# Kernel optimization log

Measured on AMD Instinct MI355X. Metric: run time of the kernel, lower is better.

## Reference

```python
import jax, jax.numpy as jnp
import numpy as np

E, T, H, I = 32, 512, 2048, 768


def setup_inputs() -> dict:
    key = jax.random.key(0)
    k1, k2, k3, k4 = jax.random.split(key, 4)
    scale = 1.0 / np.sqrt(H)
    return {
        "routed_input": jax.random.normal(k1, (E, T, H), dtype=jnp.float32),
        "gate_proj": jax.random.normal(k2, (E, I, H), dtype=jnp.float32) * scale,
        "up_proj": jax.random.normal(k3, (E, I, H), dtype=jnp.float32) * scale,
        "down_proj": jax.random.normal(k4, (E, H, I), dtype=jnp.float32) * scale,
    }


def reference(routed_input, gate_proj, up_proj, down_proj):
    # routed_input: [E, T, H]; per-expert SwiGLU MLP, concat over experts.
    gate = jnp.einsum("eth,eih->eti", routed_input, gate_proj)
    up = jnp.einsum("eth,eih->eti", routed_input, up_proj)
    hidden = jax.nn.silu(gate) * up  # [E, T, I]
    out = jnp.einsum("eti,ehi->eth", hidden, down_proj)  # [E, T, H]
    return out.reshape(E * T, H)
```

## Files before the change

### kernel.cpp

```cpp
#include <hip/hip_runtime.h>


#define NE 32
#define NT 512
#define NH 2048
#define NI 768

typedef short        short8  __attribute__((ext_vector_type(8)));
typedef float        floatx4 __attribute__((ext_vector_type(4)));
typedef unsigned int uintx2  __attribute__((ext_vector_type(2)));

__device__ __forceinline__ unsigned int cvt_pk_bf16(float lo, float hi) {
    unsigned int r;
    asm("v_cvt_pk_bf16_f32 %0, %1, %2" : "=v"(r) : "v"(lo), "v"(hi));
    return r;
}

__device__ __forceinline__ uintx2 pack4(floatx4 v) {
    uintx2 r;
    r[0] = cvt_pk_bf16(v[0], v[1]);
    r[1] = cvt_pk_bf16(v[2], v[3]);
    return r;
}

__device__ __forceinline__ ushort f2bf(float f) {
    union { float f; unsigned int u; } v; v.f = f;
    unsigned int r = v.u + 0x7fffu + ((v.u >> 16) & 1u);
    return (ushort)(r >> 16);
}

__global__ __launch_bounds__(256) void moe_gateup(
    const float* __restrict__ rin, const float* __restrict__ gate,
    const float* __restrict__ up, ushort* __restrict__ hidden)
{
    __shared__ ushort As[128][40];
    __shared__ ushort Bgs[128][40];
    __shared__ ushort Bus[128][40];

    const int bid = blockIdx.x;
    const int wg  = (bid & 7) * (768 / 8) + (bid >> 3);
    const int e   = wg / 24;
    const int rem = wg % 24;
    const int ti  = rem % 6;
    const int tm  = rem / 6;

    const int tid  = threadIdx.x;
    const int lane = tid & 63;
    const int wave = tid >> 6;
    const int wr = wave >> 1, wc = wave & 1;

    const float* Ab = rin  + (size_t)e * NT * NH + (size_t)(tm * 128) * NH;
    const float* Gb = gate + (size_t)e * NI * NH + (size_t)(ti * 128) * NH;
    const float* Ub = up   + (size_t)e * NI * NH + (size_t)(ti * 128) * NH;

    const int srow = tid >> 3;
    const int scol = (tid & 7) * 4;

    floatx4 accg[4][4], accu[4][4];
    #pragma unroll
    for (int m = 0; m < 4; ++m)
        #pragma unroll
        for (int n = 0; n < 4; ++n) {
            accg[m][n] = (floatx4)0.f;
            accu[m][n] = (floatx4)0.f;
        }

    const int frow = lane & 15;
    const int kofs = (lane >> 4) * 8;
    const int KT = NH / 32;

    floatx4 pa[4], pg[4], pu[4];
    #pragma unroll
    for (int r = 0; r < 4; ++r) {
        const size_t off = (size_t)(srow + r * 32) * NH + scol;
        pa[r] = *(const floatx4*)(Ab + off);
        pg[r] = *(const floatx4*)(Gb + off);
        pu[r] = *(const floatx4*)(Ub + off);
    }

    for (int kt = 0; kt < KT; ++kt) {
        __builtin_amdgcn_s_barrier();
        #pragma unroll
        for (int r = 0; r < 4; ++r) {
            const int row = srow + r * 32;
            *(uintx2*)&As [row][scol] = pack4(pa[r]);
            *(uintx2*)&Bgs[row][scol] = pack4(pg[r]);
            *(uintx2*)&Bus[row][scol] = pack4(pu[r]);
        }
        if (kt + 1 < KT) {
            const int k0 = (kt + 1) * 32 + scol;
            #pragma unroll
            for (int r = 0; r < 4; ++r) {
                const size_t off = (size_t)(srow + r * 32) * NH + k0;
                pa[r] = *(const floatx4*)(Ab + off);
                pg[r] = *(const floatx4*)(Gb + off);
                pu[r] = *(const floatx4*)(Ub + off);
            }
        }
        asm volatile("s_waitcnt lgkmcnt(0)" ::: "memory");
        __builtin_amdgcn_s_barrier();

        short8 af[4], gf[4], uf[4];
        #pragma unroll
        for (int m = 0; m < 4; ++m)
            af[m] = *(const short8*)&As[wr * 64 + m * 16 + frow][kofs];
        #pragma unroll
        for (int n = 0; n < 4; ++n) {
            gf[n] = *(const short8*)&Bgs[wc * 64 + n * 16 + frow][kofs];
            uf[n] = *(const short8*)&Bus[wc * 64 + n * 16 + frow][kofs];
        }
        #pragma unroll
        for (int m = 0; m < 4; ++m)
            #pragma unroll
            for (int n = 0; n < 4; ++n) {
                accg[m][n] = __builtin_amdgcn_mfma_f32_16x16x32_bf16(
                    af[m], gf[n], accg[m][n], 0, 0, 0);
                accu[m][n] = __builtin_amdgcn_mfma_f32_16x16x32_bf16(
                    af[m], uf[n], accu[m][n], 0, 0, 0);
            }
    }

    const int ccol  = lane & 15;
    const int crow0 = (lane >> 4) * 4;
    const size_t hbase = ((size_t)e * NT + (size_t)tm * 128) * NI + ti * 128;
    #pragma unroll
    for (int m = 0; m < 4; ++m)
        #pragma unroll
        for (int n = 0; n < 4; ++n)
            #pragma unroll
            for (int j = 0; j < 4; ++j) {
                const float g = accg[m][n][j];
                const float u = accu[m][n][j];
                const float h = (g / (1.f + __expf(-g))) * u;
                const int row = wr * 64 + m * 16 + crow0 + j;
                const int col = wc * 64 + n * 16 + ccol;
                hidden[hbase + (size_t)row * NI + col] = f2bf(h);
            }
}

__global__ __launch_bounds__(256) void moe_down(
    const ushort* __restrict__ hidden, const float* __restrict__ down,
    float* __restrict__ out)
{
    __shared__ ushort As[128][40];
    __shared__ ushort Bs[128][40];

    const int bid = blockIdx.x;
    const int wg  = (bid & 7) * (2048 / 8) + (bid >> 3);
    const int e   = wg >> 6;
    const int rem = wg & 63;
    const int tn  = rem & 15;
    const int tm  = rem >> 4;

    const int tid  = threadIdx.x;
    const int lane = tid & 63;
    const int wave = tid >> 6;
    const int wr = wave >> 1, wc = wave & 1;

    const ushort* Ab = hidden + ((size_t)e * NT + (size_t)tm * 128) * NI;
    const float*  Bb = down + (size_t)e * NH * NI + (size_t)(tn * 128) * NI;

    const int a_row = tid >> 2;
    const int a_col = (tid & 3) * 8;
    const int srow = tid >> 3;
    const int scol = (tid & 7) * 4;

    floatx4 acc[4][4];
    #pragma unroll
    for (int m = 0; m < 4; ++m)
        #pragma unroll
        for (int n = 0; n < 4; ++n) acc[m][n] = (floatx4)0.f;

    const int frow = lane & 15;
    const int kofs = (lane >> 4) * 8;
    const int KT = NI / 32;

    short8 pha0, pha1;
    floatx4 pb[4];
    pha0 = *(const short8*)(Ab + (size_t)a_row * NI + a_col);
    pha1 = *(const short8*)(Ab + (size_t)(a_row + 64) * NI + a_col);
    #pragma unroll
    for (int r = 0; r < 4; ++r)
        pb[r] = *(const floatx4*)(Bb + (size_t)(srow + r * 32) * NI + scol);

    for (int kt = 0; kt < KT; ++kt) {
        __builtin_amdgcn_s_barrier();
        *(short8*)&As[a_row][a_col]      = pha0;
        *(short8*)&As[a_row + 64][a_col] = pha1;
        #pragma unroll
        for (int r = 0; r < 4; ++r)
            *(uintx2*)&Bs[srow + r * 32][scol] = pack4(pb[r]);
        if (kt + 1 < KT) {
            const int k0 = (kt + 1) * 32;
            pha0 = *(const short8*)(Ab + (size_t)a_row * NI + k0 + a_col);
            pha1 = *(const short8*)(Ab + (size_t)(a_row + 64) * NI + k0 + a_col);
            #pragma unroll
            for (int r = 0; r < 4; ++r)
                pb[r] = *(const floatx4*)(Bb + (size_t)(srow + r * 32) * NI + k0 + scol);
        }
        asm volatile("s_waitcnt lgkmcnt(0)" ::: "memory");
        __builtin_amdgcn_s_barrier();

        short8 af[4], bf[4];
        #pragma unroll
        for (int m = 0; m < 4; ++m)
            af[m] = *(const short8*)&As[wr * 64 + m * 16 + frow][kofs];
        #pragma unroll
        for (int n = 0; n < 4; ++n)
            bf[n] = *(const short8*)&Bs[wc * 64 + n * 16 + frow][kofs];
        #pragma unroll
        for (int m = 0; m < 4; ++m)
            #pragma unroll
            for (int n = 0; n < 4; ++n)
                acc[m][n] = __builtin_amdgcn_mfma_f32_16x16x32_bf16(
                    af[m], bf[n], acc[m][n], 0, 0, 0);
    }

    const int ccol  = lane & 15;
    const int crow0 = (lane >> 4) * 4;
    float* Ob = out + ((size_t)e * NT + (size_t)tm * 128) * NH + tn * 128;
    #pragma unroll
    for (int m = 0; m < 4; ++m)
        #pragma unroll
        for (int n = 0; n < 4; ++n)
            #pragma unroll
            for (int j = 0; j < 4; ++j) {
                const int row = wr * 64 + m * 16 + crow0 + j;
                const int col = wc * 64 + n * 16 + ccol;
                Ob[(size_t)row * NH + col] = acc[m][n][j];
            }
}

extern "C" void kernel_launch(void* const* d_in, const int* in_sizes, int n_in,
                              void* d_out, int out_size, void* d_ws, size_t ws_size,
                              hipStream_t stream) {
    const float* rin  = (const float*)d_in[0];
    const float* gate = (const float*)d_in[1];
    const float* up   = (const float*)d_in[2];
    const float* down = (const float*)d_in[3];
    float* out = (float*)d_out;
    ushort* hidden = (ushort*)d_ws;

    dim3 blk(256);
    moe_gateup<<<dim3(768), blk, 0, stream>>>(rin, gate, up, hidden);
    moe_down<<<dim3(2048), blk, 0, stream>>>(hidden, down, out);
}
```

Baseline: 402.6 us.

## Load fp32 tiles directly into LDS via global_load_lds with XOR swizzle

Both GEMM kernels now use global_load_lds to copy fp32 (and bf16 hidden) tiles straight from global memory into LDS, with an XOR column swizzle to avoid bank conflicts. The bf16 conversion moves from the staging store to the fragment read. This removes the register staging and the separate LDS write. The register-level prefetch of the next tile is gone, so each iteration now waits on vmcnt(0) with no overlap of loads and MFMA within a block, and the larger fp32 LDS tiles may cut occupancy. Launch bounds also request 2 blocks per SIMD to recover latency hiding.

```diff
diff --git a/kernel.cpp b/kernel.cpp
--- a/kernel.cpp
+++ b/kernel.cpp
@@ -8,7 +8,12 @@
 
 typedef short        short8  __attribute__((ext_vector_type(8)));
 typedef float        floatx4 __attribute__((ext_vector_type(4)));
-typedef unsigned int uintx2  __attribute__((ext_vector_type(2)));
+typedef __attribute__((address_space(1))) const unsigned int g_u32;
+typedef __attribute__((address_space(3))) unsigned int l_u32;
+
+__device__ __forceinline__ void gl_lds16(const void* g, void* l) {
+    __builtin_amdgcn_global_load_lds((g_u32*)g, (l_u32*)l, 16, 0, 0);
+}
 
 __device__ __forceinline__ unsigned int cvt_pk_bf16(float lo, float hi) {
     unsigned int r;
@@ -16,11 +21,13 @@
     return r;
 }
 
-__device__ __forceinline__ uintx2 pack4(floatx4 v) {
-    uintx2 r;
-    r[0] = cvt_pk_bf16(v[0], v[1]);
-    r[1] = cvt_pk_bf16(v[2], v[3]);
-    return r;
+__device__ __forceinline__ short8 frag8(floatx4 x0, floatx4 x1) {
+    union { unsigned int u[4]; short8 s; } t;
+    t.u[0] = cvt_pk_bf16(x0[0], x0[1]);
+    t.u[1] = cvt_pk_bf16(x0[2], x0[3]);
+    t.u[2] = cvt_pk_bf16(x1[0], x1[1]);
+    t.u[3] = cvt_pk_bf16(x1[2], x1[3]);
+    return t.s;
 }
 
 __device__ __forceinline__ ushort f2bf(float f) {
@@ -29,13 +36,13 @@
     return (ushort)(r >> 16);
 }
 
-__global__ __launch_bounds__(256) void moe_gateup(
+__global__ __launch_bounds__(256, 2) void moe_gateup(
     const float* __restrict__ rin, const float* __restrict__ gate,
     const float* __restrict__ up, ushort* __restrict__ hidden)
 {
-    __shared__ ushort As[128][40];
-    __shared__ ushort Bgs[128][40];
-    __shared__ ushort Bus[128][40];
+    __shared__ float As[128][32];
+    __shared__ float Gs[128][32];
+    __shared__ float Us[128][32];
 
     const int bid = blockIdx.x;
     const int wg  = (bid & 7) * (768 / 8) + (bid >> 3);
@@ -53,8 +60,8 @@
     const float* Gb = gate + (size_t)e * NI * NH + (size_t)(ti * 128) * NH;
     const float* Ub = up   + (size_t)e * NI * NH + (size_t)(ti * 128) * NH;
 
-    const int srow = tid >> 3;
-    const int scol = (tid & 7) * 4;
+    const int lr = lane >> 3;
+    const int lc = lane & 7;
 
     floatx4 accg[4][4], accu[4][4];
     #pragma unroll
@@ -66,48 +73,42 @@
         }
 
     const int frow = lane & 15;
-    const int kofs = (lane >> 4) * 8;
+    const int h    = lane >> 4;
+    const int rb   = frow & 7;
+    const int c0   = (2 * h) ^ rb;
+    const int c1   = (2 * h + 1) ^ rb;
     const int KT = NH / 32;
 
-    floatx4 pa[4], pg[4], pu[4];
-    #pragma unroll
-    for (int r = 0; r < 4; ++r) {
-        const size_t off = (size_t)(srow + r * 32) * NH + scol;
-        pa[r] = *(const floatx4*)(Ab + off);
-        pg[r] = *(const floatx4*)(Gb + off);
-        pu[r] = *(const floatx4*)(Ub + off);
-    }
-
     for (int kt = 0; kt < KT; ++kt) {
-        __builtin_amdgcn_s_barrier();
-        #pragma unroll
-        for (int r = 0; r < 4; ++r) {
-            const int row = srow + r * 32;
-            *(uintx2*)&As [row][scol] = pack4(pa[r]);
-            *(uintx2*)&Bgs[row][scol] = pack4(pg[r]);
-            *(uintx2*)&Bus[row][scol] = pack4(pu[r]);
-        }
-        if (kt + 1 < KT) {
-            const int k0 = (kt + 1) * 32 + scol;
-            #pragma unroll
-            for (int r = 0; r < 4; ++r) {
-                const size_t off = (size_t)(srow + r * 32) * NH + k0;
-                pa[r] = *(const floatx4*)(Ab + off);
-                pg[r] = *(const floatx4*)(Gb + off);
-                pu[r] = *(const floatx4*)(Ub + off);
-            }
-        }
-        asm volatile("s_waitcnt lgkmcnt(0)" ::: "memory");
+        const int k0 = kt * 32;
+        __builtin_amdgcn_s_barrier();
+        #pragma unroll
+        for (int i = 0; i < 4; ++i) {
+            const int g = wave * 4 + i;
+            const int r = g * 8 + lr;
+            const int cs = lc ^ (r & 7);
+            const size_t so = (size_t)r * NH + k0 + cs * 4;
+            gl_lds16(Ab + so, &As[g * 8][0]);
+            gl_lds16(Gb + so, &Gs[g * 8][0]);
+            gl_lds16(Ub + so, &Us[g * 8][0]);
+        }
+        asm volatile("s_waitcnt vmcnt(0)" ::: "memory");
         __builtin_amdgcn_s_barrier();
 
         short8 af[4], gf[4], uf[4];
         #pragma unroll
-        for (int m = 0; m < 4; ++m)
-            af[m] = *(const short8*)&As[wr * 64 + m * 16 + frow][kofs];
+        for (int m = 0; m < 4; ++m) {
+            const int R = wr * 64 + m * 16 + frow;
+            af[m] = frag8(*(const floatx4*)&As[R][c0 * 4],
+                          *(const floatx4*)&As[R][c1 * 4]);
+        }
         #pragma unroll
         for (int n = 0; n < 4; ++n) {
-            gf[n] = *(const short8*)&Bgs[wc * 64 + n * 16 + frow][kofs];
-            uf[n] = *(const short8*)&Bus[wc * 64 + n * 16 + frow][kofs];
+            const int R = wc * 64 + n * 16 + frow;
+            gf[n] = frag8(*(const floatx4*)&Gs[R][c0 * 4],
+                          *(const floatx4*)&Gs[R][c1 * 4]);
+            uf[n] = frag8(*(const floatx4*)&Us[R][c0 * 4],
+                          *(const floatx4*)&Us[R][c1 * 4]);
         }
         #pragma unroll
         for (int m = 0; m < 4; ++m)
@@ -131,19 +132,19 @@
             for (int j = 0; j < 4; ++j) {
                 const float g = accg[m][n][j];
                 const float u = accu[m][n][j];
-                const float h = (g / (1.f + __expf(-g))) * u;
+                const float hh = (g / (1.f + __expf(-g))) * u;
                 const int row = wr * 64 + m * 16 + crow0 + j;
                 const int col = wc * 64 + n * 16 + ccol;
-                hidden[hbase + (size_t)row * NI + col] = f2bf(h);
+                hidden[hbase + (size_t)row * NI + col] = f2bf(hh);
             }
 }
 
-__global__ __launch_bounds__(256) void moe_down(
+__global__ __launch_bounds__(256, 2) void moe_down(
     const ushort* __restrict__ hidden, const float* __restrict__ down,
     float* __restrict__ out)
 {
-    __shared__ ushort As[128][40];
-    __shared__ ushort Bs[128][40];
+    __shared__ ushort As[128][32];
+    __shared__ float  Bs[128][32];
 
     const int bid = blockIdx.x;
     const int wg  = (bid & 7) * (2048 / 8) + (bid >> 3);
@@ -160,11 +161,6 @@
     const ushort* Ab = hidden + ((size_t)e * NT + (size_t)tm * 128) * NI;
     const float*  Bb = down + (size_t)e * NH * NI + (size_t)(tn * 128) * NI;
 
-    const int a_row = tid >> 2;
-    const int a_col = (tid & 3) * 8;
-    const int srow = tid >> 3;
-    const int scol = (tid & 7) * 4;
-
     floatx4 acc[4][4];
     #pragma unroll
     for (int m = 0; m < 4; ++m)
@@ -172,42 +168,45 @@
         for (int n = 0; n < 4; ++n) acc[m][n] = (floatx4)0.f;
 
     const int frow = lane & 15;
-    const int kofs = (lane >> 4) * 8;
+    const int h    = lane >> 4;
+    const int ca   = h ^ (frow & 3);
+    const int rb   = frow & 7;
+    const int c0   = (2 * h) ^ rb;
+    const int c1   = (2 * h + 1) ^ rb;
     const int KT = NI / 32;
 
-    short8 pha0, pha1;
-    floatx4 pb[4];
-    pha0 = *(const short8*)(Ab + (size_t)a_row * NI + a_col);
-    pha1 = *(const short8*)(Ab + (size_t)(a_row + 64) * NI + a_col);
-    #pragma unroll
-    for (int r = 0; r < 4; ++r)
-        pb[r] = *(const floatx4*)(Bb + (size_t)(srow + r * 32) * NI + scol);
-
     for (int kt = 0; kt < KT; ++kt) {
-        __builtin_amdgcn_s_barrier();
-        *(short8*)&As[a_row][a_col]      = pha0;
-        *(short8*)&As[a_row + 64][a_col] = pha1;
-        #pragma unroll
-        for (int r = 0; r < 4; ++r)
-            *(uintx2*)&Bs[srow + r * 32][scol] = pack4(pb[r]);
-        if (kt + 1 < KT) {
-            const int k0 = (kt + 1) * 32;
-            pha0 = *(const short8*)(Ab + (size_t)a_row * NI + k0 + a_col);
-            pha1 = *(const short8*)(Ab + (size_t)(a_row + 64) * NI + k0 + a_col);
-            #pragma unroll
-            for (int r = 0; r < 4; ++r)
-                pb[r] = *(const floatx4*)(Bb + (size_t)(srow + r * 32) * NI + k0 + scol);
-        }
-        asm volatile("s_waitcnt lgkmcnt(0)" ::: "memory");
+        const int k0 = kt * 32;
+        __builtin_amdgcn_s_barrier();
+        #pragma unroll
+        for (int i = 0; i < 2; ++i) {
+            const int g = wave * 2 + i;
+            const int r = g * 16 + (lane >> 2);
+            const int cs = (lane & 3) ^ (r & 3);
+            gl_lds16(Ab + (size_t)r * NI + k0 + cs * 8, &As[g * 16][0]);
+        }
+        #pragma unroll
+        for (int i = 0; i < 4; ++i) {
+            const int g = wave * 4 + i;
+            const int r = g * 8 + (lane >> 3);
+            const int cs = (lane & 7) ^ (r & 7);
+            gl_lds16(Bb + (size_t)r * NI + k0 + cs * 4, &Bs[g * 8][0]);
+        }
+        asm volatile("s_waitcnt vmcnt(0)" ::: "memory");
         __builtin_amdgcn_s_barrier();
 
         short8 af[4], bf[4];
         #pragma unroll
-        for (int m = 0; m < 4; ++m)
-            af[m] = *(const short8*)&As[wr * 64 + m * 16 + frow][kofs];
-        #pragma unroll
-        for (int n = 0; n < 4; ++n)
-            bf[n] = *(const short8*)&Bs[wc * 64 + n * 16 + frow][kofs];
+        for (int m = 0; m < 4; ++m) {
+            const int R = wr * 64 + m * 16 + frow;
+            af[m] = *(const short8*)&As[R][ca * 8];
+        }
+        #pragma unroll
+        for (int n = 0; n < 4; ++n) {
+            const int R = wc * 64 + n * 16 + frow;
+            bf[n] = frag8(*(const floatx4*)&Bs[R][c0 * 4],
+                          *(const floatx4*)&Bs[R][c1 * 4]);
+        }
         #pragma unroll
         for (int m = 0; m < 4; ++m)
             #pragma unroll
```

Measured after the change: 384.0 us. 1.05x faster.
